# Optimization experiments

Hardware: AMD Instinct MI355X
Metric: run time of the kernel (lower is better)

## Reference

```python
import jax, jax.numpy as jnp
import numpy as np

# BERT-base geometry
B, N, H, DH = 4, 512, 12, 64
HID = H * DH            # 768
E = 65536               # total edges (~avg degree 32)
NREL = 64               # relation vocabulary


def setup_inputs() -> dict:
    key = jax.random.key(0)
    ks = jax.random.split(key, 12)
    node_states = jax.random.normal(ks[0], (B, N, HID), jnp.float32)
    b = jax.random.randint(ks[1], (E,), 0, B)
    hn = jax.random.randint(ks[2], (E,), 0, N)
    tn = jax.random.randint(ks[3], (E,), 0, N)
    r = jax.random.randint(ks[4], (E,), 0, NREL)
    edge_indices = jnp.stack([b, hn, tn, r]).astype(jnp.int32)  # (4, E)
    node_type_ids = jnp.zeros((B, N), jnp.int32)  # unused by this subclass
    sc = 0.02
    Wq = jax.random.normal(ks[5], (HID, HID), jnp.float32) * sc
    bq = jnp.zeros((HID,), jnp.float32)
    Wk = jax.random.normal(ks[6], (HID, HID), jnp.float32) * sc
    bk = jnp.zeros((HID,), jnp.float32)
    Wv = jax.random.normal(ks[7], (HID, HID), jnp.float32) * sc
    bv = jnp.zeros((HID,), jnp.float32)
    # relation matrix embeddings: one (DH, DH) matrix per relation id
    rel_emb = jnp.eye(DH, dtype=jnp.float32)[None] + jax.random.normal(ks[8], (NREL, DH, DH), jnp.float32) * sc
    return {"node_states": node_states, "edge_indices": edge_indices,
            "node_type_ids": node_type_ids, "Wq": Wq, "bq": bq,
            "Wk": Wk, "bk": bk, "Wv": Wv, "bv": bv, "rel_emb": rel_emb}


def reference(node_states, edge_indices, node_type_ids, Wq, bq, Wk, bk, Wv, bv, rel_emb):
    Bq, Nn, hid = node_states.shape
    # dense QKV projections (torch Linear: y = x @ W^T + b)
    Q = node_states @ Wq.T + bq
    K = node_states @ Wk.T + bk
    V = (node_states @ Wv.T + bv).reshape(Bq, Nn, H, DH)  # (B,N,H,D)
    be, he, te, re = edge_indices  # each (E,)
    # per-edge gathers
    Qe = Q[be, he].reshape(-1, H, DH)   # (E,H,D)
    Ke = K[be, te].reshape(-1, H, DH)   # (E,H,D)
    Re = rel_emb[re]                     # (E,D,D) relation matrix per edge
    # Q projected through relation matrix, then inner product with K per head
    Qp = jnp.einsum('ehd,edk->ehk', Qe, Re)
    logits = jnp.einsum('ehd,ehd->eh', Qp, Ke) / jnp.sqrt(jnp.float32(DH))  # (E,H)
    # sparse softmax over tail nodes: segment = (batch, head_node)
    seg = be * Nn + he
    nseg = Bq * Nn
    m = jax.ops.segment_max(logits, seg, num_segments=nseg)      # (BN,H)
    ex = jnp.exp(logits - m[seg])
    denom = jax.ops.segment_sum(ex, seg, num_segments=nseg)      # (BN,H)
    p = ex / denom[seg]                                          # (E,H)
    # dropout prob = 0.0 (deterministic reference)
    # aggregate: out[b,i,h,:] = sum_edges p_e * V[b, tail_e, h, :]
    contrib = p[:, :, None] * V[be, te]                          # (E,H,D)
    out = jax.ops.segment_sum(contrib, seg, num_segments=nseg)   # (BN,H,D)
    return out.reshape(Bq, Nn, H * DH)
```

## Files before the change

### kernel.cpp

```cpp
#include <hip/hip_runtime.h>
#include <hip/hip_bf16.h>

#define NB   4
#define NN   512
#define NH   12
#define DHD  64
#define HID  768
#define NE   65536
#define NSEG 2048
#define NREL 64
#define LGS  16
#define SCAP 128
#define NSUB2 8
#define RSUB (NREL * NSUB2)
#define RCAP 256
#define RLY2 2
#define POISON 0xAAAAAAAAu

typedef short bf16x8 __attribute__((ext_vector_type(8)));
typedef float f32x4  __attribute__((ext_vector_type(4)));
typedef unsigned short u16x8 __attribute__((ext_vector_type(8)));

__device__ __forceinline__ unsigned short f2bf(float f) {
    __hip_bfloat16 h = __float2bfloat16(f);
    return *reinterpret_cast<unsigned short*>(&h);
}
__device__ __forceinline__ float bf2f(unsigned short s) {
    return __int_as_float(((int)s) << 16);
}
__device__ __forceinline__ int unpz(int v) {
    return (int)((unsigned)v - POISON);
}
__device__ __forceinline__ void load_lds16(const void* g, void* l) {
    __builtin_amdgcn_global_load_lds(
        (const __attribute__((address_space(1))) unsigned int*)g,
        (__attribute__((address_space(3))) unsigned int*)l, 16, 0, 0);
}

#define NX4 ((2048 * 768) / 4)
#define NW4 ((768 * 768) / 4)
#define NCAST ((NX4 + 3 * NW4) / 256)
__global__ __launch_bounds__(256) void cast_scatter_kernel(
    const float* __restrict__ X, const float* __restrict__ Wq,
    const float* __restrict__ Wk, const float* __restrict__ Wv,
    unsigned short* __restrict__ Xh, unsigned short* __restrict__ Wh,
    const int* __restrict__ ei,
    int* __restrict__ cursor, int* __restrict__ rcursor,
    int* __restrict__ s_te, int* __restrict__ s_pkr)
{
    if (blockIdx.x >= NCAST) {
        const int e = (blockIdx.x - NCAST) * 256 + threadIdx.x;
        const int b  = ei[e];
        const int hn = ei[NE + e];
        const int tn = ei[2 * NE + e];
        const int rr = ei[3 * NE + e];
        const int seg = b * NN + hn;
        const int slot = unpz(atomicAdd(&cursor[seg], 1)) & (SCAP - 1);
        const int pos  = seg * SCAP + slot;
        s_te[pos] = tn;
        const int rsub = rr * NSUB2 + ((e >> 8) & (NSUB2 - 1));
        const int rj = unpz(atomicAdd(&rcursor[rsub], 1)) & (RCAP - 1);
        int2 pv2; pv2.x = (seg << 9) | tn; pv2.y = pos;
        ((int2*)s_pkr)[rsub * RCAP + rj] = pv2;
        return;
    }
    const int i = blockIdx.x * 256 + threadIdx.x;
    float4 v;
    ushort4* dst;
    if (i < NX4) {
        v = ((const float4*)X)[i];
        dst = &((ushort4*)Xh)[i];
    } else {
        const int j = i - NX4;
        const float* W = (j < NW4) ? Wq : ((j < 2 * NW4) ? Wk : Wv);
        const int jj = (j < NW4) ? j : ((j < 2 * NW4) ? j - NW4 : j - 2 * NW4);
        v = ((const float4*)W)[jj];
        dst = &((ushort4*)Wh)[j];
    }
    ushort4 r;
    r.x = f2bf(v.x); r.y = f2bf(v.y); r.z = f2bf(v.z); r.w = f2bf(v.w);
    *dst = r;
}

#define NQKV 576
__global__ __launch_bounds__(256) void qkv_kernel(
    const unsigned short* __restrict__ Xh, const unsigned short* __restrict__ Wh,
    const float* __restrict__ bq, const float* __restrict__ bk,
    const float* __restrict__ bv,
    unsigned short* __restrict__ Qh, unsigned short* __restrict__ Kh,
    unsigned short* __restrict__ Vh)
{
    __shared__ __align__(16) char smem[64 * 132 * 4];
    const int tid = threadIdx.x;

    const int gb  = blockIdx.x;
    const int bid = (gb & 7) * 72 + (gb >> 3);
    const int z   = bid / 192;
    const int rem = bid - z * 192;
    const int by  = rem / 6;
    const int bx  = rem - by * 6;
    const unsigned short* W = Wh + (size_t)z * (768 * 768);
    const float* bias = (z == 0) ? bq : ((z == 1) ? bk : bv);

    const int n0 = bx * 128;
    const int m0 = by * 64;
    const int lane = tid & 63;
    const int wave = tid >> 6;
    const int wm = wave >> 1, wn = wave & 1;

    unsigned short* As = (unsigned short*)smem;
    unsigned short* Bs = (unsigned short*)(smem + 8192);
    float* Cs = (float*)smem;

    f32x4 acc[2][4];
    #pragma unroll
    for (int a = 0; a < 2; ++a)
        #pragma unroll
        for (int b2 = 0; b2 < 4; ++b2) acc[a][b2] = (f32x4){0.f, 0.f, 0.f, 0.f};

    const int ml = lane & 15;
    const int q4 = lane >> 4;

    for (int k0 = 0; k0 < HID; k0 += 64) {
        __syncthreads();
        #pragma unroll
        for (int i = 0; i < 2; ++i) {
            const int slotb = i * 256 + wave * 64;
            const int idx = slotb + lane;
            const int row = idx >> 3;
            const int kq  = (idx & 7) ^ (row & 7);
            load_lds16(Xh + (size_t)(m0 + row) * HID + k0 + kq * 8,
                       As + slotb * 8);
        }
        #pragma unroll
        for (int i = 0; i < 4; ++i) {
            const int slotb = i * 256 + wave * 64;
            const int idx = slotb + lane;
            const int row = idx >> 3;
            const int kq  = (idx & 7) ^ (row & 7);
            load_lds16(W + (size_t)(n0 + row) * HID + k0 + kq * 8,
                       Bs + slotb * 8);
        }
        __syncthreads();

        #pragma unroll
        for (int ks = 0; ks < 2; ++ks) {
            bf16x8 af[2], bfr[4];
            #pragma unroll
            for (int t = 0; t < 2; ++t) {
                const int ar = wm * 32 + t * 16 + ml;
                const int ac = (ks * 4 + q4) ^ (ar & 7);
                af[t] = *(const bf16x8*)(As + ar * 64 + ac * 8);
            }
            #pragma unroll
            for (int t = 0; t < 4; ++t) {
                const int br = wn * 64 + t * 16 + ml;
                const int bc = (ks * 4 + q4) ^ (br & 7);
                bfr[t] = *(const bf16x8*)(Bs + br * 64 + bc * 8);
            }
            #pragma unroll
            for (int mt = 0; mt < 2; ++mt)
                #pragma unroll
                for (int nt = 0; nt < 4; ++nt)
                    acc[mt][nt] = __builtin_amdgcn_mfma_f32_16x16x32_bf16(
                        af[mt], bfr[nt], acc[mt][nt], 0, 0, 0);
        }
    }

    __syncthreads();
    #pragma unroll
    for (int mt = 0; mt < 2; ++mt)
        #pragma unroll
        for (int nt = 0; nt < 4; ++nt)
            #pragma unroll
            for (int rg = 0; rg < 4; ++rg)
                Cs[(wm * 32 + mt * 16 + q4 * 4 + rg) * 132 +
                   wn * 64 + nt * 16 + ml] = acc[mt][nt][rg];
    __syncthreads();

    unsigned short* Y = (z == 0) ? Qh : ((z == 1) ? Kh : Vh);
    #pragma unroll
    for (int it = 0; it < 4; ++it) {
        const int id  = tid + it * 256;
        const int row = id >> 4;
        const int cg  = id & 15;
        const float* cp = Cs + row * 132 + cg * 8;
        const float4 cA = *(const float4*)cp;
        const float4 cB = *(const float4*)(cp + 4);
        const float* bp = bias + n0 + cg * 8;
        const float4 bA = *(const float4*)bp;
        const float4 bB = *(const float4*)(bp + 4);
        const size_t o = (size_t)(m0 + row) * HID + n0 + cg * 8;
        u16x8 r;
        r[0] = f2bf(cA.x + bA.x); r[1] = f2bf(cA.y + bA.y);
        r[2] = f2bf(cA.z + bA.z); r[3] = f2bf(cA.w + bA.w);
        r[4] = f2bf(cB.x + bB.x); r[5] = f2bf(cB.y + bB.y);
        r[6] = f2bf(cB.z + bB.z); r[7] = f2bf(cB.w + bB.w);
        *(u16x8*)&Y[o] = r;
    }
}

__global__ __launch_bounds__(256) void rel_logits(
    const unsigned short* __restrict__ Qh, const unsigned short* __restrict__ Kh,
    const float* __restrict__ rel,
    const int* __restrict__ rcursor, const int* __restrict__ s_pkr,
    float* __restrict__ Lg)
{
    const int rs = blockIdx.x;
    int cnt = unpz(rcursor[rs]);
    cnt = (cnt < 0) ? 0 : ((cnt > RCAP) ? RCAP : cnt);
    const int rows = cnt * NH;
    if ((int)blockIdx.y * 256 >= rows) return;
    const int r = rs >> 3;
    const int tid = threadIdx.x;
    const int lane = tid & 63;
    const int wave = tid >> 6;

    __shared__ int qb[256], kb[256], oi[256];
    __shared__ float QpS[4][16][68];
    __shared__ __align__(16) unsigned short frS[4096];

    {
        const float* Rg = rel + (size_t)r * 4096;
        #pragma unroll
        for (int it = 0; it < 4; ++it) {
            const int i4 = it * 256 + tid;
            const float4 v4 = ((const float4*)Rg)[i4];
            const int d  = i4 >> 4;
            const int c0 = (i4 & 15) * 4;
            const int ks = d >> 5, q4 = (d >> 3) & 3, j = d & 7;
            const float vv[4] = {v4.x, v4.y, v4.z, v4.w};
            #pragma unroll
            for (int e = 0; e < 4; ++e) {
                const int c = c0 + e, nt = c >> 4, n = c & 15;
                frS[((ks * 4 + nt) * 64 + q4 * 16 + n) * 8 + j] = f2bf(vv[e]);
            }
        }
    }
    __syncthreads();
    bf16x8 bfrag[2][4];
    #pragma unroll
    for (int ks = 0; ks < 2; ++ks)
        #pragma unroll
        for (int nt = 0; nt < 4; ++nt)
            bfrag[ks][nt] = *(const bf16x8*)(frS + ((ks * 4 + nt) * 64 + lane) * 8);

    for (int t0 = blockIdx.y * 256; t0 < rows; t0 += RLY2 * 256) {
        __syncthreads();
        {
            const int rowid = t0 + tid;
            if (rowid < rows) {
                const int el = rowid / 12;
                const int h  = rowid - el * 12;
                const int2 v = ((const int2*)s_pkr)[rs * RCAP + el];
                const int pos = v.y & (NSEG * SCAP - 1);
                const int sg  = (v.x >> 9) & (NSEG - 1);
                const int te  = v.x & (NN - 1);
                qb[tid] = sg * HID + h * 64;
                kb[tid] = ((sg & ~(NN - 1)) + te) * HID + h * 64;
                oi[tid] = pos * LGS + h;
            } else { qb[tid] = 0; kb[tid] = 0; oi[tid] = -1; }
        }
        __syncthreads();

        const int rw = lane >> 2, ch = (lane & 3) * 16;
        bf16x8 kv0[4], kv1[4];
        #pragma unroll
        for (int gi = 0; gi < 4; ++gi) {
            const int kbase = kb[(wave + gi * 4) * 16 + rw];
            kv0[gi] = *(const bf16x8*)(Kh + kbase + ch);
            kv1[gi] = *(const bf16x8*)(Kh + kbase + ch + 8);
        }

        #pragma unroll
        for (int gi = 0; gi < 4; ++gi) {
            const int g = wave + gi * 4;
            const int m = lane & 15, q4 = lane >> 4;
            const int qbase = qb[g * 16 + m];
            f32x4 cfr[4] = {{0,0,0,0},{0,0,0,0},{0,0,0,0},{0,0,0,0}};
            #pragma unroll
            for (int ks = 0; ks < 2; ++ks) {
                const bf16x8 afr = *(const bf16x8*)(Qh + qbase + ks * 32 + q4 * 8);
                #pragma unroll
                for (int nt = 0; nt < 4; ++nt)
                    cfr[nt] = __builtin_amdgcn_mfma_f32_16x16x32_bf16(
                        afr, bfrag[ks][nt], cfr[nt], 0, 0, 0);
            }
            #pragma unroll
            for (int nt = 0; nt < 4; ++nt)
                #pragma unroll
                for (int rg = 0; rg < 4; ++rg)
                    QpS[wave][q4 * 4 + rg][nt * 16 + m] = cfr[nt][rg];

            const int rowid2 = g * 16 + rw;
            float s = 0.f;
            #pragma unroll
            for (int i = 0; i < 8; ++i) {
                s = fmaf(QpS[wave][rw][ch + i],     bf2f((unsigned short)kv0[gi][i]), s);
                s = fmaf(QpS[wave][rw][ch + 8 + i], bf2f((unsigned short)kv1[gi][i]), s);
            }
            s += __shfl_xor(s, 1, 64);
            s += __shfl_xor(s, 2, 64);
            if ((lane & 3) == 0) {
                const int o = oi[rowid2];
                if (o >= 0) Lg[o] = __expf(s * 0.125f);
            }
        }
    }
}

__global__ __launch_bounds__(256) void seg_softmax_agg(
    const unsigned short* __restrict__ Vh, const float* __restrict__ Lg,
    const int* __restrict__ s_te,
    float* __restrict__ out,
    int* __restrict__ cursor, int* __restrict__ rcursor)
{
    const int tid  = threadIdx.x;
    const int lane = tid & 63;
    const int w    = tid >> 6;
    const int seg  = blockIdx.x * 4 + w;

    int cnt = unpz(cursor[seg]);
    __syncthreads();
    if (tid < 4) cursor[blockIdx.x * 4 + tid] = (int)POISON;
    if (blockIdx.x < RSUB / 4 && tid < 4)
        rcursor[blockIdx.x * 4 + tid] = (int)POISON;
    cnt = (cnt < 0) ? 0 : ((cnt > SCAP) ? SCAP : cnt);

    const int base = seg * SCAP;
    const int browbase = seg & ~(NN - 1);
    const int h0 = lane >> 4;

    __shared__ float pjS[4][12][68];
    __shared__ int   teS[4][64];

    float4 acc[3] = {{0,0,0,0},{0,0,0,0},{0,0,0,0}};
    float dl[12];
    #pragma unroll
    for (int h = 0; h < 12; ++h) dl[h] = 0.f;

    for (int c0 = 0; c0 < cnt; c0 += 64) {
        const int cc = min(64, cnt - c0);
        float4 pA = {0,0,0,0}, pB = {0,0,0,0}, pC = {0,0,0,0};
        int te = 0;
        if (lane < cc) {
            const float* Lp = Lg + (size_t)(base + c0 + lane) * LGS;
            pA = *(const float4*)(Lp);
            pB = *(const float4*)(Lp + 4);
            pC = *(const float4*)(Lp + 8);
            te = s_te[base + c0 + lane] & (NN - 1);
        }
        teS[w][lane] = te;
        pjS[w][0][lane]  = pA.x; pjS[w][1][lane]  = pA.y;
        pjS[w][2][lane]  = pA.z; pjS[w][3][lane]  = pA.w;
        pjS[w][4][lane]  = pB.x; pjS[w][5][lane]  = pB.y;
        pjS[w][6][lane]  = pB.z; pjS[w][7][lane]  = pB.w;
        pjS[w][8][lane]  = pC.x; pjS[w][9][lane]  = pC.y;
        pjS[w][10][lane] = pC.z; pjS[w][11][lane] = pC.w;
        dl[0] += pA.x; dl[1] += pA.y; dl[2]  += pA.z; dl[3]  += pA.w;
        dl[4] += pB.x; dl[5] += pB.y; dl[6]  += pB.z; dl[7]  += pB.w;
        dl[8] += pC.x; dl[9] += pC.y; dl[10] += pC.z; dl[11] += pC.w;

        for (int j = 0; j < cc; ++j) {
            const int row = browbase + teS[w][j];
            const unsigned short* Vr = Vh + (size_t)row * HID + (lane << 2);
            const ushort4 v0 = *(const ushort4*)(Vr);
            const ushort4 v1 = *(const ushort4*)(Vr + 256);
            const ushort4 v2 = *(const ushort4*)(Vr + 512);
            const float p0 = pjS[w][h0][j];
            const float p1 = pjS[w][4 + h0][j];
            const float p2 = pjS[w][8 + h0][j];
            acc[0].x = fmaf(p0, bf2f(v0.x), acc[0].x);
            acc[0].y = fmaf(p0, bf2f(v0.y), acc[0].y);
            acc[0].z = fmaf(p0, bf2f(v0.z), acc[0].z);
            acc[0].w = fmaf(p0, bf2f(v0.w), acc[0].w);
            acc[1].x = fmaf(p1, bf2f(v1.x), acc[1].x);
            acc[1].y = fmaf(p1, bf2f(v1.y), acc[1].y);
            acc[1].z = fmaf(p1, bf2f(v1.z), acc[1].z);
            acc[1].w = fmaf(p1, bf2f(v1.w), acc[1].w);
            acc[2].x = fmaf(p2, bf2f(v2.x), acc[2].x);
            acc[2].y = fmaf(p2, bf2f(v2.y), acc[2].y);
            acc[2].z = fmaf(p2, bf2f(v2.z), acc[2].z);
            acc[2].w = fmaf(p2, bf2f(v2.w), acc[2].w);
        }
    }

    #pragma unroll
    for (int o = 1; o < 64; o <<= 1) {
        #pragma unroll
        for (int h = 0; h < 12; ++h) dl[h] += __shfl_xor(dl[h], o, 64);
    }
    float* Yo = out + (size_t)seg * HID + (lane << 2);
    #pragma unroll
    for (int k = 0; k < 3; ++k) {
        const float d = dl[k * 4 + h0];
        float4 r;
        r.x = (d > 0.f) ? acc[k].x / d : 0.f;
        r.y = (d > 0.f) ? acc[k].y / d : 0.f;
        r.z = (d > 0.f) ? acc[k].z / d : 0.f;
        r.w = (d > 0.f) ? acc[k].w / d : 0.f;
        *(float4*)(Yo + k * 256) = r;
    }
}

extern "C" void kernel_launch(void* const* d_in, const int* in_sizes, int n_in,
                              void* d_out, int out_size, void* d_ws, size_t ws_size,
                              hipStream_t stream)
{
    const float* X   = (const float*)d_in[0];
    const int*   EI  = (const int*)d_in[1];
    const float* Wq  = (const float*)d_in[3];
    const float* bq  = (const float*)d_in[4];
    const float* Wk  = (const float*)d_in[5];
    const float* bk  = (const float*)d_in[6];
    const float* Wv  = (const float*)d_in[7];
    const float* bv  = (const float*)d_in[8];
    const float* rel = (const float*)d_in[9];
    float* out = (float*)d_out;

    char* p = (char*)d_ws;
    unsigned short* Qh = (unsigned short*)p;  p += (size_t)NSEG * HID * 2;
    unsigned short* Kh = (unsigned short*)p;  p += (size_t)NSEG * HID * 2;
    unsigned short* Vh = (unsigned short*)p;  p += (size_t)NSEG * HID * 2;
    float* Lg = (float*)p;                    p += (size_t)NSEG * SCAP * LGS * 4;
    unsigned short* Xh = (unsigned short*)p;  p += (size_t)NB * NN * HID * 2;
    unsigned short* Wh = (unsigned short*)p;  p += (size_t)3 * 768 * 768 * 2;
    int* cursor   = (int*)p;                  p += NSEG * 4;
    int* rcursor  = (int*)p;                  p += RSUB * 4;
    int* s_te     = (int*)p;                  p += (size_t)NSEG * SCAP * 4;
    int* s_pkr    = (int*)p;                  p += (size_t)RSUB * RCAP * 8;

    cast_scatter_kernel<<<NCAST + 256, 256, 0, stream>>>(
        X, Wq, Wk, Wv, Xh, Wh, EI, cursor, rcursor, s_te, s_pkr);
    qkv_kernel<<<NQKV, 256, 0, stream>>>(
        Xh, Wh, bq, bk, bv, Qh, Kh, Vh);
    rel_logits<<<dim3(RSUB, RLY2), 256, 0, stream>>>(
        Qh, Kh, rel, rcursor, s_pkr, Lg);
    seg_softmax_agg<<<NSEG / 4, 256, 0, stream>>>(
        Vh, Lg, s_te, out, cursor, rcursor);
}
```

Before: 166.5 us.

## Double-buffer LDS tiles in QKV GEMM to overlap global loads with MFMA

```diff
diff --git a/kernel.cpp b/kernel.cpp
--- a/kernel.cpp
+++ b/kernel.cpp
@@ -90,7 +90,7 @@
     unsigned short* __restrict__ Qh, unsigned short* __restrict__ Kh,
     unsigned short* __restrict__ Vh)
 {
-    __shared__ __align__(16) char smem[64 * 132 * 4];
+    __shared__ __align__(16) char smem[49152];
     const int tid = threadIdx.x;
 
     const int gb  = blockIdx.x;
@@ -108,8 +108,6 @@
     const int wave = tid >> 6;
     const int wm = wave >> 1, wn = wave & 1;
 
-    unsigned short* As = (unsigned short*)smem;
-    unsigned short* Bs = (unsigned short*)(smem + 8192);
     float* Cs = (float*)smem;
 
     f32x4 acc[2][4];
@@ -121,28 +119,50 @@
     const int ml = lane & 15;
     const int q4 = lane >> 4;
 
+    int offA[2], offB[4];
+    #pragma unroll
+    for (int i = 0; i < 2; ++i) {
+        const int idx = i * 256 + wave * 64 + lane;
+        const int row = idx >> 3;
+        const int kq  = (idx & 7) ^ (row & 7);
+        offA[i] = (m0 + row) * HID + kq * 8;
+    }
+    #pragma unroll
+    for (int i = 0; i < 4; ++i) {
+        const int idx = i * 256 + wave * 64 + lane;
+        const int row = idx >> 3;
+        const int kq  = (idx & 7) ^ (row & 7);
+        offB[i] = (n0 + row) * HID + kq * 8;
+    }
+
+    #pragma unroll
+    for (int i = 0; i < 2; ++i)
+        load_lds16(Xh + offA[i],
+                   (unsigned short*)smem + (i * 256 + wave * 64) * 8);
+    #pragma unroll
+    for (int i = 0; i < 4; ++i)
+        load_lds16(W + offB[i],
+                   (unsigned short*)(smem + 8192) + (i * 256 + wave * 64) * 8);
+    __syncthreads();
+
+    int cur = 0;
     for (int k0 = 0; k0 < HID; k0 += 64) {
-        __syncthreads();
-        #pragma unroll
-        for (int i = 0; i < 2; ++i) {
-            const int slotb = i * 256 + wave * 64;
-            const int idx = slotb + lane;
-            const int row = idx >> 3;
-            const int kq  = (idx & 7) ^ (row & 7);
-            load_lds16(Xh + (size_t)(m0 + row) * HID + k0 + kq * 8,
-                       As + slotb * 8);
-        }
-        #pragma unroll
-        for (int i = 0; i < 4; ++i) {
-            const int slotb = i * 256 + wave * 64;
-            const int idx = slotb + lane;
-            const int row = idx >> 3;
-            const int kq  = (idx & 7) ^ (row & 7);
-            load_lds16(W + (size_t)(n0 + row) * HID + k0 + kq * 8,
-                       Bs + slotb * 8);
-        }
-        __syncthreads();
-
+        const int nxt = cur ^ 1;
+        if (k0 + 64 < HID) {
+            unsigned short* An = (unsigned short*)(smem + nxt * 24576);
+            unsigned short* Bn = (unsigned short*)(smem + nxt * 24576 + 8192);
+            #pragma unroll
+            for (int i = 0; i < 2; ++i)
+                load_lds16(Xh + offA[i] + k0 + 64,
+                           An + (i * 256 + wave * 64) * 8);
+            #pragma unroll
+            for (int i = 0; i < 4; ++i)
+                load_lds16(W + offB[i] + k0 + 64,
+                           Bn + (i * 256 + wave * 64) * 8);
+        }
+        const unsigned short* Ac = (const unsigned short*)(smem + cur * 24576);
+        const unsigned short* Bc =
+            (const unsigned short*)(smem + cur * 24576 + 8192);
         #pragma unroll
         for (int ks = 0; ks < 2; ++ks) {
             bf16x8 af[2], bfr[4];
@@ -150,13 +170,13 @@
             for (int t = 0; t < 2; ++t) {
                 const int ar = wm * 32 + t * 16 + ml;
                 const int ac = (ks * 4 + q4) ^ (ar & 7);
-                af[t] = *(const bf16x8*)(As + ar * 64 + ac * 8);
+                af[t] = *(const bf16x8*)(Ac + ar * 64 + ac * 8);
             }
             #pragma unroll
             for (int t = 0; t < 4; ++t) {
                 const int br = wn * 64 + t * 16 + ml;
                 const int bc = (ks * 4 + q4) ^ (br & 7);
-                bfr[t] = *(const bf16x8*)(Bs + br * 64 + bc * 8);
+                bfr[t] = *(const bf16x8*)(Bc + br * 64 + bc * 8);
             }
             #pragma unroll
             for (int mt = 0; mt < 2; ++mt)
@@ -165,9 +185,10 @@
                     acc[mt][nt] = __builtin_amdgcn_mfma_f32_16x16x32_bf16(
                         af[mt], bfr[nt], acc[mt][nt], 0, 0, 0);
         }
-    }
-
-    __syncthreads();
+        __syncthreads();
+        cur = nxt;
+    }
+
     #pragma unroll
     for (int mt = 0; mt < 2; ++mt)
         #pragma unroll
```

Measured after the change: 165.1 us. Within noise of the previous version (-0.8%).
